# Performance work log

Hardware: AMD Instinct MI355X
Metric: run time of the kernel (lower is better)

The kernel has to match this reference:

```python
import jax, jax.numpy as jnp
import numpy as np

COMMITMENT_COST = 0.25
NUM_EMBEDDINGS = 1024
EMBEDDING_DIM = 512  # win_size(8) * num_pellets(64)


def setup_inputs() -> dict:
    key = jax.random.key(0)
    k1, k2 = jax.random.split(key)
    inputs = jax.random.normal(k1, (64, 256, EMBEDDING_DIM), dtype=jnp.float32)
    # matches torch init: uniform_(-1/K, 1/K)
    lim = 1.0 / NUM_EMBEDDINGS
    emb_weight = jax.random.uniform(k2, (NUM_EMBEDDINGS, EMBEDDING_DIM),
                                    dtype=jnp.float32, minval=-lim, maxval=lim)
    return {"inputs": inputs, "emb_weight": emb_weight}


def reference(inputs, emb_weight):
    batch_size = inputs.shape[0]
    input_shape = inputs.shape
    flat = inputs.reshape(-1, EMBEDDING_DIM)  # [N, D]

    distances = (jnp.sum(flat * flat, axis=1, keepdims=True)
                 + jnp.sum(emb_weight * emb_weight, axis=1)
                 - 2.0 * flat @ emb_weight.T)
    encoding_indices = jnp.argmin(distances, axis=1)  # [N]

    # gather instead of one-hot matmul (same math)
    quantized = emb_weight[encoding_indices].reshape(input_shape)

    e_latent_loss = jnp.mean((jax.lax.stop_gradient(quantized) - inputs) ** 2)
    q_latent_loss = jnp.mean((quantized - jax.lax.stop_gradient(inputs)) ** 2)
    loss_vq = q_latent_loss + COMMITMENT_COST * e_latent_loss

    # straight-through estimator
    quantized = inputs + jax.lax.stop_gradient(quantized - inputs)

    encoding_indices = encoding_indices.reshape(batch_size, -1)
    return loss_vq, quantized, encoding_indices
```

## Files before the change

kernel.cpp:

```cpp
#include <hip/hip_runtime.h>
#include <cfloat>

#define NROWS  16384
#define DIM    512
#define KC     1024
#define QELEMS (NROWS * DIM)

#define NSPLIT 8

typedef float  floatx4 __attribute__((ext_vector_type(4)));
typedef _Float16 half8 __attribute__((ext_vector_type(8)));
typedef _Float16 half4 __attribute__((ext_vector_type(4)));

__device__ __forceinline__ void gl_lds16(const _Float16* g, void* l) {
    __builtin_amdgcn_global_load_lds(
        (const __attribute__((address_space(1))) unsigned int*)g,
        (__attribute__((address_space(3))) unsigned int*)l,
        16, 0, 0);
}

__global__ __launch_bounds__(256) void prep_kernel(const float* __restrict__ A,
                                                   const float* __restrict__ E,
                                                   float* __restrict__ xsq,
                                                   float* __restrict__ esq,
                                                   _Float16* __restrict__ ah,
                                                   _Float16* __restrict__ al,
                                                   _Float16* __restrict__ eh,
                                                   _Float16* __restrict__ el,
                                                   unsigned long long* __restrict__ packed,
                                                   float* __restrict__ out) {
    if (blockIdx.x == 0 && threadIdx.x == 0) out[0] = 0.f;
    const int wave = threadIdx.x >> 6, lane = threadIdx.x & 63;
    const bool isA = blockIdx.x < (NROWS / 4);
    const int row = (isA ? blockIdx.x : blockIdx.x - NROWS / 4) * 4 + wave;
    const float* M = isA ? A : E;
    const float scale = isA ? 2048.0f : 65536.0f;

    const float4* Mr = (const float4*)(M + (size_t)row * DIM);
    float4 va = Mr[lane];
    float4 vb = Mr[lane + 64];
    float s = 0.f;
    s += va.x*va.x + va.y*va.y + va.z*va.z + va.w*va.w;
    s += vb.x*vb.x + vb.y*vb.y + vb.z*vb.z + vb.w*vb.w;
    #pragma unroll
    for (int off = 32; off; off >>= 1) s += __shfl_down(s, off, 64);
    if (lane == 0) {
        if (isA) { xsq[row] = s; packed[row] = ~0ULL; }
        else     { esq[row] = s; }
    }

    float xa[4] = {va.x, va.y, va.z, va.w}, xb[4] = {vb.x, vb.y, vb.z, vb.w};
    half4 ha, la, hb, lb;
    #pragma unroll
    for (int e = 0; e < 4; ++e) {
        float t = xa[e] * scale;
        _Float16 h = (_Float16)t;
        ha[e] = h; la[e] = (_Float16)(t - (float)h);
        t = xb[e] * scale;
        h = (_Float16)t;
        hb[e] = h; lb[e] = (_Float16)(t - (float)h);
    }
    _Float16* hr = (isA ? ah : eh) + (size_t)row * DIM;
    _Float16* lr = (isA ? al : el) + (size_t)row * DIM;
    ((half4*)hr)[lane]      = ha;
    ((half4*)lr)[lane]      = la;
    ((half4*)hr)[lane + 64] = hb;
    ((half4*)lr)[lane + 64] = lb;
}

__global__ __launch_bounds__(256) void mfma_argmin_kernel(const _Float16* __restrict__ ah,
                                                          const _Float16* __restrict__ al,
                                                          const _Float16* __restrict__ eh,
                                                          const _Float16* __restrict__ el,
                                                          const float* __restrict__ esq,
                                                          const float* __restrict__ xsq,
                                                          unsigned long long* __restrict__ packed) {
    __shared__ half8 AhT[2][512], AlT[2][512], EhT[2][512], ElT[2][512];
    __shared__ float redv[128][2];
    __shared__ int   redi[128][2];

    const int tid = threadIdx.x;
    const int lane = tid & 63, wave = tid >> 6;
    const int wm = wave >> 1, wn = wave & 1;
    const int tx = lane & 15, qd = lane >> 4;
    const int bm = blockIdx.x & 127, bn = blockIdx.x >> 7;
    const int m0 = bm * 128, c0 = bn * 128;

    const int rowL = (wave & 1) * 64 + lane;
    const int kqL  = wave >> 1;
    size_t offA = (size_t)(m0 + rowL) * DIM + kqL * 8;
    size_t offE = (size_t)(c0 + rowL) * DIM + kqL * 8;
    const int cb0 = wave * 64, cb1 = 256 + wave * 64;

    floatx4 acc[4][4];
    #pragma unroll
    for (int i = 0; i < 4; ++i)
        #pragma unroll
        for (int j = 0; j < 4; ++j) acc[i][j] = (floatx4){0.f, 0.f, 0.f, 0.f};

    gl_lds16(ah + offA,      &AhT[0][cb0]);
    gl_lds16(ah + offA + 16, &AhT[0][cb1]);
    gl_lds16(al + offA,      &AlT[0][cb0]);
    gl_lds16(al + offA + 16, &AlT[0][cb1]);
    gl_lds16(eh + offE,      &EhT[0][cb0]);
    gl_lds16(eh + offE + 16, &EhT[0][cb1]);
    gl_lds16(el + offE,      &ElT[0][cb0]);
    gl_lds16(el + offE + 16, &ElT[0][cb1]);
    offA += 32; offE += 32;
    __syncthreads();

    #pragma unroll 1
    for (int kt = 0; kt < DIM / 32; ++kt) {
        const int cur = kt & 1, nxt = cur ^ 1;
        if (kt < DIM / 32 - 1) {
            gl_lds16(ah + offA,      &AhT[nxt][cb0]);
            gl_lds16(ah + offA + 16, &AhT[nxt][cb1]);
            gl_lds16(al + offA,      &AlT[nxt][cb0]);
            gl_lds16(al + offA + 16, &AlT[nxt][cb1]);
            gl_lds16(eh + offE,      &EhT[nxt][cb0]);
            gl_lds16(eh + offE + 16, &EhT[nxt][cb1]);
            gl_lds16(el + offE,      &ElT[nxt][cb0]);
            gl_lds16(el + offE + 16, &ElT[nxt][cb1]);
            offA += 32; offE += 32;
        }

        half8 fa[4], fbh[4], fbl[4];
        #pragma unroll
        for (int i = 0; i < 4; ++i)
            fa[i] = AhT[cur][qd * 128 + wm * 64 + i * 16 + tx];
        #pragma unroll
        for (int j = 0; j < 4; ++j) {
            fbh[j] = EhT[cur][qd * 128 + wn * 64 + j * 16 + tx];
            fbl[j] = ElT[cur][qd * 128 + wn * 64 + j * 16 + tx];
        }
        #pragma unroll
        for (int i = 0; i < 4; ++i)
            #pragma unroll
            for (int j = 0; j < 4; ++j)
                acc[i][j] = __builtin_amdgcn_mfma_f32_16x16x32_f16(fa[i], fbh[j], acc[i][j], 0, 0, 0);
        #pragma unroll
        for (int i = 0; i < 4; ++i)
            #pragma unroll
            for (int j = 0; j < 4; ++j)
                acc[i][j] = __builtin_amdgcn_mfma_f32_16x16x32_f16(fa[i], fbl[j], acc[i][j], 0, 0, 0);
        #pragma unroll
        for (int i = 0; i < 4; ++i)
            fa[i] = AlT[cur][qd * 128 + wm * 64 + i * 16 + tx];
        #pragma unroll
        for (int i = 0; i < 4; ++i)
            #pragma unroll
            for (int j = 0; j < 4; ++j)
                acc[i][j] = __builtin_amdgcn_mfma_f32_16x16x32_f16(fa[i], fbh[j], acc[i][j], 0, 0, 0);

        __syncthreads();
    }

    float sqe_v[4];
    #pragma unroll
    for (int j = 0; j < 4; ++j) sqe_v[j] = esq[c0 + wn * 64 + j * 16 + tx];
    #pragma unroll
    for (int i = 0; i < 4; ++i) {
        #pragma unroll
        for (int r = 0; r < 4; ++r) {
            int rl = wm * 64 + i * 16 + qd * 4 + r;
            float sx = xsq[m0 + rl];
            float bvv = FLT_MAX; int bii = 0x7fffffff;
            #pragma unroll
            for (int j = 0; j < 4; ++j) {
                float S = sx + sqe_v[j];
                float s = S - acc[i][j][r] * (1.0f / 67108864.0f);
                int c = c0 + wn * 64 + j * 16 + tx;
                if (s < bvv || (s == bvv && c < bii)) { bvv = s; bii = c; }
            }
            #pragma unroll
            for (int md = 1; md < 16; md <<= 1) {
                float ov = __shfl_xor(bvv, md, 64);
                int   oc = __shfl_xor(bii, md, 64);
                if (ov < bvv || (ov == bvv && oc < bii)) { bvv = ov; bii = oc; }
            }
            if (tx == 0) { redv[rl][wn] = bvv; redi[rl][wn] = bii; }
        }
    }
    __syncthreads();
    if (tid < 128) {
        float v0 = redv[tid][0], v1 = redv[tid][1];
        int   i0 = redi[tid][0], i1 = redi[tid][1];
        float v = (v1 < v0) ? v1 : v0;
        int   ix = (v1 < v0) ? i1 : i0;
        unsigned long long pk = ((unsigned long long)__float_as_uint(v) << 32)
                              | (unsigned int)ix;
        atomicMin(&packed[m0 + tid], pk);
    }
}

__global__ __launch_bounds__(256) void finalize_kernel(const float* __restrict__ A,
                                                       const float* __restrict__ E,
                                                       const unsigned long long* __restrict__ packed,
                                                       float* __restrict__ out) {
    float* q = out + 1;
    float* idxF = out + 1 + QELEMS;
    const int tid = threadIdx.x;
    const int r0 = blockIdx.x * 32;

    __shared__ int sidx[32];
    if (tid < 32) {
        int idx = (int)(unsigned int)(packed[r0 + tid] & 0xFFFFFFFFull);
        sidx[tid] = idx;
        idxF[r0 + tid] = (float)idx;
    }
    __syncthreads();

    float sacc = 0.f;
    #pragma unroll 4
    for (int it = 0; it < 16; ++it) {
        int flat = it * 256 + tid;
        int row = flat >> 7;
        int d4  = (flat & 127) * 4;
        int idx = sidx[row];
        float4 e = *(const float4*)(E + (size_t)idx * DIM + d4);
        float4 x = *(const float4*)(A + (size_t)(r0 + row) * DIM + d4);
        *(float4*)(q + (size_t)(r0 + row) * DIM + d4) = e;
        float d0 = e.x - x.x, d1 = e.y - x.y, d2 = e.z - x.z, d3 = e.w - x.w;
        sacc += d0*d0 + d1*d1 + d2*d2 + d3*d3;
    }
    #pragma unroll
    for (int off = 32; off; off >>= 1) sacc += __shfl_down(sacc, off, 64);
    __shared__ float ps[4];
    if ((tid & 63) == 0) ps[tid >> 6] = sacc;
    __syncthreads();
    if (tid == 0)
        atomicAdd(out, (ps[0] + ps[1] + ps[2] + ps[3]) * (1.25f / (float)QELEMS));
}

extern "C" void kernel_launch(void* const* d_in, const int* in_sizes, int n_in,
                              void* d_out, int out_size, void* d_ws, size_t ws_size,
                              hipStream_t stream) {
    const float* A = (const float*)d_in[0];
    const float* E = (const float*)d_in[1];
    float* out = (float*)d_out;

    unsigned long long* packed = (unsigned long long*)d_ws;
    float*    esq  = (float*)(packed + NROWS);
    float*    xsq  = esq + KC;
    _Float16* eh   = (_Float16*)(xsq + NROWS);
    _Float16* el   = eh + (size_t)KC * DIM;
    _Float16* ah   = el + (size_t)KC * DIM;
    _Float16* al   = ah + (size_t)NROWS * DIM;

    prep_kernel<<<NROWS / 4 + KC / 4, 256, 0, stream>>>(A, E, xsq, esq, ah, al, eh, el, packed, out);
    mfma_argmin_kernel<<<(NROWS / 128) * NSPLIT, 256, 0, stream>>>(
        ah, al, eh, el, esq, xsq, packed);
    finalize_kernel<<<NROWS / 32, 256, 0, stream>>>(A, E, packed, out);
}
```

Baseline: 191.6 us.

## Stage GEMM tiles via registers with padded LDS; derive loss from argmin distances

The distance GEMM now loads fp16 tiles into registers and stores them into padded LDS buffers, replacing direct global-to-LDS loads, to reduce bank conflicts and overlap loads with MFMA work. The finalize kernel stops rereading the inputs and computes the loss by summing the minimum distances already stored in the packed argmin words. This removes a full pass over the input tensor. The trade-off is that the loss inherits the cancellation error of the expanded-distance formula.

```diff
diff --git a/kernel.cpp b/kernel.cpp
--- a/kernel.cpp
+++ b/kernel.cpp
@@ -7,17 +7,11 @@
 #define QELEMS (NROWS * DIM)
 
 #define NSPLIT 8
+#define CHUNKS 132
 
 typedef float  floatx4 __attribute__((ext_vector_type(4)));
 typedef _Float16 half8 __attribute__((ext_vector_type(8)));
 typedef _Float16 half4 __attribute__((ext_vector_type(4)));
-
-__device__ __forceinline__ void gl_lds16(const _Float16* g, void* l) {
-    __builtin_amdgcn_global_load_lds(
-        (const __attribute__((address_space(1))) unsigned int*)g,
-        (__attribute__((address_space(3))) unsigned int*)l,
-        16, 0, 0);
-}
 
 __global__ __launch_bounds__(256) void prep_kernel(const float* __restrict__ A,
                                                    const float* __restrict__ E,
@@ -75,7 +69,8 @@
                                                           const float* __restrict__ esq,
                                                           const float* __restrict__ xsq,
                                                           unsigned long long* __restrict__ packed) {
-    __shared__ half8 AhT[2][512], AlT[2][512], EhT[2][512], ElT[2][512];
+    __shared__ half8 AhT[2][4 * CHUNKS], AlT[2][4 * CHUNKS];
+    __shared__ half8 EhT[2][4 * CHUNKS], ElT[2][4 * CHUNKS];
     __shared__ float redv[128][2];
     __shared__ int   redi[128][2];
 
@@ -86,11 +81,12 @@
     const int bm = blockIdx.x & 127, bn = blockIdx.x >> 7;
     const int m0 = bm * 128, c0 = bn * 128;
 
-    const int rowL = (wave & 1) * 64 + lane;
-    const int kqL  = wave >> 1;
-    size_t offA = (size_t)(m0 + rowL) * DIM + kqL * 8;
-    size_t offE = (size_t)(c0 + rowL) * DIM + kqL * 8;
-    const int cb0 = wave * 64, cb1 = 256 + wave * 64;
+    const int srow = tid >> 2, skq = tid & 3;
+    const _Float16* gA  = ah + (size_t)(m0 + srow) * DIM + skq * 8;
+    const _Float16* gAl = al + (size_t)(m0 + srow) * DIM + skq * 8;
+    const _Float16* gE  = eh + (size_t)(c0 + srow) * DIM + skq * 8;
+    const _Float16* gEl = el + (size_t)(c0 + srow) * DIM + skq * 8;
+    const int cw0 = skq * CHUNKS + srow, cw1 = cw0 + 64;
 
     floatx4 acc[4][4];
     #pragma unroll
@@ -98,40 +94,43 @@
         #pragma unroll
         for (int j = 0; j < 4; ++j) acc[i][j] = (floatx4){0.f, 0.f, 0.f, 0.f};
 
-    gl_lds16(ah + offA,      &AhT[0][cb0]);
-    gl_lds16(ah + offA + 16, &AhT[0][cb1]);
-    gl_lds16(al + offA,      &AlT[0][cb0]);
-    gl_lds16(al + offA + 16, &AlT[0][cb1]);
-    gl_lds16(eh + offE,      &EhT[0][cb0]);
-    gl_lds16(eh + offE + 16, &EhT[0][cb1]);
-    gl_lds16(el + offE,      &ElT[0][cb0]);
-    gl_lds16(el + offE + 16, &ElT[0][cb1]);
-    offA += 32; offE += 32;
-    __syncthreads();
+    half8 rA0  = *(const half8*)(gA);
+    half8 rA1  = *(const half8*)(gA  + 64 * DIM);
+    half8 rL0  = *(const half8*)(gAl);
+    half8 rL1  = *(const half8*)(gAl + 64 * DIM);
+    half8 rE0  = *(const half8*)(gE);
+    half8 rE1  = *(const half8*)(gE  + 64 * DIM);
+    half8 rF0  = *(const half8*)(gEl);
+    half8 rF1  = *(const half8*)(gEl + 64 * DIM);
+    AhT[0][cw0] = rA0; AhT[0][cw1] = rA1;
+    AlT[0][cw0] = rL0; AlT[0][cw1] = rL1;
+    EhT[0][cw0] = rE0; EhT[0][cw1] = rE1;
+    ElT[0][cw0] = rF0; ElT[0][cw1] = rF1;
 
     #pragma unroll 1
     for (int kt = 0; kt < DIM / 32; ++kt) {
         const int cur = kt & 1, nxt = cur ^ 1;
+        const int kb = (kt + 1) * 32;
         if (kt < DIM / 32 - 1) {
-            gl_lds16(ah + offA,      &AhT[nxt][cb0]);
-            gl_lds16(ah + offA + 16, &AhT[nxt][cb1]);
-            gl_lds16(al + offA,      &AlT[nxt][cb0]);
-            gl_lds16(al + offA + 16, &AlT[nxt][cb1]);
-            gl_lds16(eh + offE,      &EhT[nxt][cb0]);
-            gl_lds16(eh + offE + 16, &EhT[nxt][cb1]);
-            gl_lds16(el + offE,      &ElT[nxt][cb0]);
-            gl_lds16(el + offE + 16, &ElT[nxt][cb1]);
-            offA += 32; offE += 32;
-        }
+            rA0 = *(const half8*)(gA  + kb);
+            rA1 = *(const half8*)(gA  + 64 * DIM + kb);
+            rL0 = *(const half8*)(gAl + kb);
+            rL1 = *(const half8*)(gAl + 64 * DIM + kb);
+            rE0 = *(const half8*)(gE  + kb);
+            rE1 = *(const half8*)(gE  + 64 * DIM + kb);
+            rF0 = *(const half8*)(gEl + kb);
+            rF1 = *(const half8*)(gEl + 64 * DIM + kb);
+        }
+        __syncthreads();
 
         half8 fa[4], fbh[4], fbl[4];
         #pragma unroll
         for (int i = 0; i < 4; ++i)
-            fa[i] = AhT[cur][qd * 128 + wm * 64 + i * 16 + tx];
+            fa[i] = AhT[cur][qd * CHUNKS + wm * 64 + i * 16 + tx];
         #pragma unroll
         for (int j = 0; j < 4; ++j) {
-            fbh[j] = EhT[cur][qd * 128 + wn * 64 + j * 16 + tx];
-            fbl[j] = ElT[cur][qd * 128 + wn * 64 + j * 16 + tx];
+            fbh[j] = EhT[cur][qd * CHUNKS + wn * 64 + j * 16 + tx];
+            fbl[j] = ElT[cur][qd * CHUNKS + wn * 64 + j * 16 + tx];
         }
         #pragma unroll
         for (int i = 0; i < 4; ++i)
@@ -145,14 +144,19 @@
                 acc[i][j] = __builtin_amdgcn_mfma_f32_16x16x32_f16(fa[i], fbl[j], acc[i][j], 0, 0, 0);
         #pragma unroll
         for (int i = 0; i < 4; ++i)
-            fa[i] = AlT[cur][qd * 128 + wm * 64 + i * 16 + tx];
+            fa[i] = AlT[cur][qd * CHUNKS + wm * 64 + i * 16 + tx];
         #pragma unroll
         for (int i = 0; i < 4; ++i)
             #pragma unroll
             for (int j = 0; j < 4; ++j)
                 acc[i][j] = __builtin_amdgcn_mfma_f32_16x16x32_f16(fa[i], fbh[j], acc[i][j], 0, 0, 0);
 
-        __syncthreads();
+        if (kt < DIM / 32 - 1) {
+            AhT[nxt][cw0] = rA0; AhT[nxt][cw1] = rA1;
+            AlT[nxt][cw0] = rL0; AlT[nxt][cw1] = rL1;
+            EhT[nxt][cw0] = rE0; EhT[nxt][cw1] = rE1;
+            ElT[nxt][cw0] = rF0; ElT[nxt][cw1] = rF1;
+        }
     }
 
     float sqe_v[4];
@@ -193,43 +197,36 @@
     }
 }
 
-__global__ __launch_bounds__(256) void finalize_kernel(const float* __restrict__ A,
-                                                       const float* __restrict__ E,
+__global__ __launch_bounds__(256) void finalize_kernel(const float* __restrict__ E,
                                                        const unsigned long long* __restrict__ packed,
                                                        float* __restrict__ out) {
     float* q = out + 1;
     float* idxF = out + 1 + QELEMS;
     const int tid = threadIdx.x;
-    const int r0 = blockIdx.x * 32;
-
-    __shared__ int sidx[32];
-    if (tid < 32) {
-        int idx = (int)(unsigned int)(packed[r0 + tid] & 0xFFFFFFFFull);
+    const int r0 = blockIdx.x * 64;
+
+    __shared__ int sidx[64];
+    if (tid < 64) {
+        unsigned long long pk = packed[r0 + tid];
+        int idx = (int)(unsigned int)(pk & 0xFFFFFFFFull);
+        float sc = __uint_as_float((unsigned int)(pk >> 32));
         sidx[tid] = idx;
         idxF[r0 + tid] = (float)idx;
+        #pragma unroll
+        for (int off = 32; off; off >>= 1) sc += __shfl_down(sc, off, 64);
+        if (tid == 0) atomicAdd(out, sc * (1.25f / (float)QELEMS));
     }
     __syncthreads();
 
-    float sacc = 0.f;
     #pragma unroll 4
-    for (int it = 0; it < 16; ++it) {
+    for (int it = 0; it < 32; ++it) {
         int flat = it * 256 + tid;
         int row = flat >> 7;
         int d4  = (flat & 127) * 4;
         int idx = sidx[row];
         float4 e = *(const float4*)(E + (size_t)idx * DIM + d4);
-        float4 x = *(const float4*)(A + (size_t)(r0 + row) * DIM + d4);
         *(float4*)(q + (size_t)(r0 + row) * DIM + d4) = e;
-        float d0 = e.x - x.x, d1 = e.y - x.y, d2 = e.z - x.z, d3 = e.w - x.w;
-        sacc += d0*d0 + d1*d1 + d2*d2 + d3*d3;
-    }
-    #pragma unroll
-    for (int off = 32; off; off >>= 1) sacc += __shfl_down(sacc, off, 64);
-    __shared__ float ps[4];
-    if ((tid & 63) == 0) ps[tid >> 6] = sacc;
-    __syncthreads();
-    if (tid == 0)
-        atomicAdd(out, (ps[0] + ps[1] + ps[2] + ps[3]) * (1.25f / (float)QELEMS));
+    }
 }
 
 extern "C" void kernel_launch(void* const* d_in, const int* in_sizes, int n_in,
@@ -250,5 +247,5 @@
     prep_kernel<<<NROWS / 4 + KC / 4, 256, 0, stream>>>(A, E, xsq, esq, ah, al, eh, el, packed, out);
     mfma_argmin_kernel<<<(NROWS / 128) * NSPLIT, 256, 0, stream>>>(
         ah, al, eh, el, esq, xsq, packed);
-    finalize_kernel<<<NROWS / 32, 256, 0, stream>>>(A, E, packed, out);
-}
+    finalize_kernel<<<NROWS / 64, 256, 0, stream>>>(E, packed, out);
+}
```

After: 167.3 us. 12.7% less time.
